# Performance work log

Measured on AMD Instinct MI355X. Metric: run time of the kernel, lower is better.

Reference implementation:

```python
import jax, jax.numpy as jnp
import numpy as np

NUM_CLASSES = 80
STRIDES = (8, 16, 32)
FEAT_HW = ((80, 80), (40, 40), (20, 20))
B = 32
MAX_GT = 60


def setup_inputs() -> dict:
    key = jax.random.key(0)
    ks = jax.random.split(key, 6)
    feats = {}
    for i, (s, (h, w)) in enumerate(zip(STRIDES, FEAT_HW)):
        feats[f"feat{s}"] = jax.random.normal(ks[i], (B, 5 + NUM_CLASSES, h, w), jnp.float32)
    u = jax.random.uniform(ks[3], (B, MAX_GT, 4), jnp.float32)
    # cx,cy in [0,640), w,h in [8,128): realistic pixel-space gt boxes for a 640x640 image
    gt_boxes = jnp.concatenate([u[..., :2] * 640.0, u[..., 2:] * 120.0 + 8.0], -1)
    gt_classes = jax.random.randint(ks[4], (B, MAX_GT), 0, NUM_CLASSES)
    num_gts = jax.random.randint(ks[5], (B,), 1, MAX_GT + 1)
    return dict(feat8=feats["feat8"], feat16=feats["feat16"], feat32=feats["feat32"],
                gt_boxes=gt_boxes, gt_classes=gt_classes, num_gts=num_gts)


def _decode(feat, stride):
    # torch get_output_and_grid: xy=(raw+grid)*stride, wh=exp(raw)*stride
    b, c, h, w = feat.shape
    yv, xv = jnp.meshgrid(jnp.arange(h), jnp.arange(w), indexing="ij")
    gx = xv.reshape(-1).astype(feat.dtype)  # [H*W]
    gy = yv.reshape(-1).astype(feat.dtype)
    out = feat.reshape(b, c, h * w).transpose(0, 2, 1)  # [B,A,C]
    xy = (out[..., :2] + jnp.stack([gx, gy], -1)[None]) * stride
    wh = jnp.exp(out[..., 2:4]) * stride
    return jnp.concatenate([xy, wh, out[..., 4:]], -1), gx, gy


def _pair_iou(a, b):
    # a: [G,4] xywh, b: [A,4] xywh -> [G,A] IoU (bboxes_iou, xyxy=False)
    tl = jnp.maximum(a[:, None, :2] - a[:, None, 2:] * 0.5, b[None, :, :2] - b[None, :, 2:] * 0.5)
    br = jnp.minimum(a[:, None, :2] + a[:, None, 2:] * 0.5, b[None, :, :2] + b[None, :, 2:] * 0.5)
    en = jnp.all(tl < br, -1)
    inter = jnp.where(en, jnp.prod(br - tl, -1), 0.0)
    area_a = jnp.prod(a[:, 2:], -1)
    area_b = jnp.prod(b[:, 2:], -1)
    return inter / (area_a[:, None] + area_b[None, :] - inter + 1e-16)


def _bce_logits(x, t):
    return jnp.maximum(x, 0.0) - x * t + jnp.log1p(jnp.exp(-jnp.abs(x)))


def _iou_loss(pred, tgt):
    # IOUloss(loss_type='iou'): 1 - iou^2, per box
    tl = jnp.maximum(pred[..., :2] - pred[..., 2:] * 0.5, tgt[..., :2] - tgt[..., 2:] * 0.5)
    br = jnp.minimum(pred[..., :2] + pred[..., 2:] * 0.5, tgt[..., :2] + tgt[..., 2:] * 0.5)
    en = jnp.all(tl < br, -1)
    inter = jnp.where(en, jnp.prod(br - tl, -1), 0.0)
    union = jnp.prod(pred[..., 2:], -1) + jnp.prod(tgt[..., 2:], -1) - inter
    iou = inter / (union + 1e-16)
    return 1.0 - iou ** 2


def _assign(boxes, cls_lo, obj_lo, gtb, gtc, vmask, cx, cy, st):
    # SimOTA per image. boxes [A,4], cls_lo [A,C], obj_lo [A], gtb [G,4], gtc [G] int,
    # vmask [G] bool (gt padding), cx/cy/st [A] anchor centers & strides.
    G, A = gtb.shape[0], boxes.shape[0]
    iou = _pair_iou(gtb, boxes)  # [G,A]
    gx, gy = gtb[:, :1], gtb[:, 1:2]
    gw, gh = gtb[:, 2:3], gtb[:, 3:4]
    in_box = ((cx[None] > gx - 0.5 * gw) & (cx[None] < gx + 0.5 * gw) &
              (cy[None] > gy - 0.5 * gh) & (cy[None] < gy + 0.5 * gh))
    R = 2.5  # center sampling radius (in strides)
    in_ctr = ((cx[None] > gx - R * st[None]) & (cx[None] < gx + R * st[None]) &
              (cy[None] > gy - R * st[None]) & (cy[None] < gy + R * st[None]))
    fg = ((in_box | in_ctr) & vmask[:, None]).any(0)  # [A] candidate anchors
    in_both = (in_box & in_ctr).astype(boxes.dtype)
    # pairwise cls cost: BCE(sqrt(sig(cls)*sig(obj)), onehot(gt_cls)).sum(-1),
    # decomposed to avoid the [G,A,C] tensor: sum_c bce0 + (bce1-bce0)[gt_cls]
    p = jnp.clip(jnp.sqrt(jax.nn.sigmoid(cls_lo) * jax.nn.sigmoid(obj_lo)[:, None]), 1e-7, 1.0 - 1e-7)
    bce1 = -jnp.log(p)          # [A,C]
    bce0 = -jnp.log(1.0 - p)    # [A,C]
    cls_cost = bce0.sum(-1)[None, :] + (bce1 - bce0)[:, gtc].T  # [G,A]
    cost = (cls_cost + 3.0 * (-jnp.log(iou + 1e-8))
            + 100000.0 * (1.0 - in_both)
            + 1e9 * (~fg)[None, :].astype(boxes.dtype)
            + 1e9 * (~vmask)[:, None].astype(boxes.dtype))
    K = 10  # n_candidate_k
    topk_ious, _ = jax.lax.top_k(iou * fg[None, :], K)
    dyn_k = jnp.maximum(topk_ious.sum(-1).astype(jnp.int32), 1)  # clamp(int(sum), min=1)
    _, pos = jax.lax.top_k(-cost, K)  # [G,K] lowest-cost anchors per gt
    sel = (jnp.arange(K)[None, :] < dyn_k[:, None]).astype(boxes.dtype)
    matching = jnp.zeros((G, A), boxes.dtype).at[jnp.arange(G)[:, None], pos].set(sel)
    matching = matching * vmask[:, None].astype(boxes.dtype)
    # resolve anchors claimed by >1 gt: keep min-cost gt
    conflict = matching.sum(0) > 1
    best_gt = jnp.argmin(cost, axis=0)  # [A]
    matching = jnp.where(conflict[None, :], jax.nn.one_hot(best_gt, G, dtype=matching.dtype).T, matching)
    fg_final = matching.sum(0) > 0  # [A]
    matched = jnp.argmax(matching, axis=0)  # [A]
    pred_iou = (matching * iou).sum(0)  # [A]
    cls_t = jax.nn.one_hot(gtc[matched], NUM_CLASSES, dtype=boxes.dtype) * pred_iou[:, None]
    reg_t = gtb[matched]
    return fg_final, cls_t, reg_t


def _forward(feat8, feat16, feat32, gt_boxes, gt_classes, num_gts):
    outs, cxs, cys, sts = [], [], [], []
    for f, s in zip((feat8, feat16, feat32), STRIDES):
        o, gx, gy = _decode(f, float(s))
        outs.append(o)
        cxs.append((gx + 0.5) * s)
        cys.append((gy + 0.5) * s)
        sts.append(jnp.full_like(gx, s))
    preds = jnp.concatenate(outs, 1)  # [B,A,5+C]
    cx = jnp.concatenate(cxs)
    cy = jnp.concatenate(cys)
    st = jnp.concatenate(sts)
    boxes = preds[..., :4]
    obj_lo = preds[..., 4]
    cls_lo = preds[..., 5:]
    vmask = jnp.arange(MAX_GT)[None, :] < num_gts[:, None]
    fg, cls_t, reg_t = jax.vmap(_assign, in_axes=(0, 0, 0, 0, 0, 0, None, None, None))(
        boxes, cls_lo, obj_lo, gt_boxes, gt_classes, vmask, cx, cy, st)
    # SimOTA assignment is no_grad in YOLOX: targets are constants wrt preds
    fg = jax.lax.stop_gradient(fg)
    cls_t = jax.lax.stop_gradient(cls_t)
    reg_t = jax.lax.stop_gradient(reg_t)
    fg_f = fg.astype(boxes.dtype)
    num_fg = jnp.maximum(fg_f.sum(), 1.0)
    loss_iou = (_iou_loss(boxes, reg_t) * fg_f).sum()
    loss_obj = _bce_logits(obj_lo, fg_f * 0.9).sum()  # obj_targets * 0.9 smoothing
    loss_cls = (_bce_logits(cls_lo, cls_t) * fg_f[..., None]).sum()
    REG_WEIGHT = 5.0
    return (REG_WEIGHT * loss_iou + loss_obj + loss_cls) / num_fg


def reference(feat8, feat16, feat32, gt_boxes, gt_classes, num_gts):
    return _forward(feat8, feat16, feat32, gt_boxes, gt_classes, num_gts)
```

## Files before the change

kernel.cpp:

```cpp
#include <hip/hip_runtime.h>

constexpr int kB = 32;
constexpr int kA = 8400;
constexpr int kG = 60;
constexpr int kC = 80;
constexpr int kK = 10;
constexpr int kNBx = (kA + 255)/256;
constexpr int kNB = kNBx * kB;

__device__ __forceinline__ float fexp(float x){ return __expf(x); }
__device__ __forceinline__ float flog(float x){ return __logf(x); }
__device__ __forceinline__ float frcp(float x){ return __builtin_amdgcn_rcpf(x); }
__device__ __forceinline__ float frsq(float x){ return __builtin_amdgcn_rsqf(x); }
__device__ __forceinline__ float fsqrt(float x){ return __builtin_amdgcn_sqrtf(x); }
__device__ __forceinline__ float fdiv(float a, float b){ return a * __builtin_amdgcn_rcpf(b); }
__device__ __forceinline__ float sigm(float x){ return frcp(1.0f + fexp(-x)); }
__device__ __forceinline__ float bce(float x, float t){
  return fmaxf(x, 0.0f) - x*t + flog(1.0f + fexp(-fabsf(x)));
}

__device__ __forceinline__ unsigned ordbits(float v){
  unsigned u = __float_as_uint(v);
  return (u & 0x80000000u) ? ~u : (u | 0x80000000u);
}
__device__ __forceinline__ float unpackf(unsigned k){
  return __uint_as_float((k & 0x80000000u) ? (k & 0x7fffffffu) : ~k);
}

struct AInfo { int x, y; float st; };
__device__ __forceinline__ AInfo ainfo(int a){
  AInfo r;
  if (a < 6400)      { r.x = a % 80;           r.y = a / 80;           r.st = 8.0f;  }
  else if (a < 8000) { int l = a-6400; r.x = l % 40; r.y = l / 40;     r.st = 16.0f; }
  else               { int l = a-8000; r.x = l % 20; r.y = l / 20;     r.st = 32.0f; }
  return r;
}

__device__ __forceinline__ float featv(const float* __restrict__ f8,
                                       const float* __restrict__ f16,
                                       const float* __restrict__ f32x,
                                       int b, int ch, int a){
  if (a < 6400) return f8 [(b*85 + ch)*6400 + a];
  if (a < 8000) return f16[(b*85 + ch)*1600 + (a - 6400)];
  return             f32x[(b*85 + ch)*400  + (a - 8000)];
}

__device__ __forceinline__ float pair_iou(float4 g, float4 p){
  float tlx = fmaxf(g.x - g.z*0.5f, p.x - p.z*0.5f);
  float tly = fmaxf(g.y - g.w*0.5f, p.y - p.w*0.5f);
  float brx = fminf(g.x + g.z*0.5f, p.x + p.z*0.5f);
  float bry = fminf(g.y + g.w*0.5f, p.y + p.w*0.5f);
  float inter = (tlx < brx && tly < bry) ? (brx-tlx)*(bry-tly) : 0.0f;
  return fdiv(inter, g.z*g.w + p.z*p.w - inter + 1e-16f);
}

__device__ __forceinline__ float cost_core(float iou, float cl, float obs, float b0sum,
                                           int a, float4 gt, int fg_a){
  AInfo ai = ainfo(a);
  float cx = ((float)ai.x + 0.5f)*ai.st;
  float cy = ((float)ai.y + 0.5f)*ai.st;
  bool in_box = (cx > gt.x - 0.5f*gt.z) && (cx < gt.x + 0.5f*gt.z)
             && (cy > gt.y - 0.5f*gt.w) && (cy < gt.y + 0.5f*gt.w);
  bool in_ctr = (cx > gt.x - 2.5f*ai.st) && (cx < gt.x + 2.5f*ai.st)
             && (cy > gt.y - 2.5f*ai.st) && (cy < gt.y + 2.5f*ai.st);
  float p = fsqrt(sigm(cl) * obs);
  p = fminf(fmaxf(p, 1e-7f), 1.0f - 1e-7f);
  float diff = -flog(p) + flog(1.0f - p);
  float c = b0sum + diff;
  c += 3.0f * (-flog(iou + 1e-8f));
  c += (in_box && in_ctr) ? 0.0f : 100000.0f;
  c += fg_a ? 0.0f : 1000000000.0f;
  return c;
}

__device__ __forceinline__ unsigned long long wave_max64(unsigned long long v){
  #pragma unroll
  for (int off = 32; off; off >>= 1){
    unsigned long long o = __shfl_xor(v, off, 64);
    if (o > v) v = o;
  }
  return v;
}

__device__ __forceinline__ void stage16(const float* g, float* l){
  __builtin_amdgcn_global_load_lds(
      (const __attribute__((address_space(1))) void*)g,
      (__attribute__((address_space(3))) void*)l, 16, 0, 0);
}
__device__ __forceinline__ void wait_vm6(int n){
  if      (n >= 6) asm volatile("s_waitcnt vmcnt(6)" ::: "memory");
  else if (n >= 4) asm volatile("s_waitcnt vmcnt(4)" ::: "memory");
  else if (n >= 2) asm volatile("s_waitcnt vmcnt(2)" ::: "memory");
  else             asm volatile("s_waitcnt vmcnt(0)" ::: "memory");
  __builtin_amdgcn_sched_barrier(0);
}

__global__ __launch_bounds__(256) void k_decode(
    const float* __restrict__ f8, const float* __restrict__ f16, const float* __restrict__ f32x,
    const float* __restrict__ gtb, const int* __restrict__ ngts,
    float* __restrict__ boxes, float* __restrict__ boxesZ,
    float* __restrict__ objl, float* __restrict__ b0s,
    float* __restrict__ bceS, float* __restrict__ obsA,
    int* __restrict__ fg, int* __restrict__ cnt, int* __restrict__ mtch){
  int b = blockIdx.y;
  int tid = threadIdx.x;
  int lane = tid & 63, wid = tid >> 6;
  int a0 = blockIdx.x*256 + tid;
  bool alive = (a0 < kA);
  int a = alive ? a0 : (kA - 1);
  __shared__ float4 sg[kG];
  __shared__ float buf[4][8][4][64];
  if (tid < kG) sg[tid] = ((const float4*)gtb)[b*kG + tid];
  int ng = ngts[b];
  __syncthreads();

  const float* base; int hw, off; float st_; int gx, gy;
  if (a < 6400)      { base=f8;   hw=6400; off=a;        st_=8.0f;  gx=off%80; gy=off/80; }
  else if (a < 8000) { base=f16;  hw=1600; off=a-6400;   st_=16.0f; gx=off%40; gy=off/40; }
  else               { base=f32x; hw=400;  off=a-8000;   st_=32.0f; gx=off%20; gy=off/20; }
  const float* p0 = base + ((size_t)b*85)*hw + off;

  int aw = blockIdx.x*256 + wid*64;
  const float* wbasep; int whw, woff;
  if (aw < 6400)      { wbasep=f8;   whw=6400; woff=aw;        }
  else if (aw < 8000) { wbasep=f16;  whw=1600; woff=aw-6400;   }
  else                { wbasep=f32x; whw=400;  woff=aw-8000;   }
  int cl4 = lane >> 4;
  int m4  = (lane & 15) << 2;
  int mo  = woff + m4; if (mo > whw - 4) mo = whw - 4;
  const float* srcb = wbasep + ((size_t)b*85 + 5)*whw + mo;
  float* ldst = &buf[wid][0][0][0];

  float t0 = p0[0];
  float t1 = p0[(size_t)hw];
  float t2 = p0[(size_t)2*hw];
  float t3 = p0[(size_t)3*hw];
  float ob = p0[(size_t)4*hw];
  __builtin_amdgcn_sched_barrier(0);
  #pragma unroll
  for (int u = 0; u < 8; ++u)
    stage16(srcb + (size_t)(4*u + cl4)*whw, ldst + u*256);
  __builtin_amdgcn_sched_barrier(0);

  float4 bx;
  bx.x = (t0 + (float)gx) * st_;
  bx.y = (t1 + (float)gy) * st_;
  bx.z = fexp(t2) * st_;
  bx.w = fexp(t3) * st_;
  float obs = sigm(ob);
  float so = fsqrt(obs);
  float cx = ((float)gx + 0.5f)*st_;
  float cy = ((float)gy + 0.5f)*st_;
  int f = 0;
  for (int g = 0; g < ng; ++g){
    float4 gt = sg[g];
    bool in_box = (cx > gt.x - 0.5f*gt.z) && (cx < gt.x + 0.5f*gt.z)
               && (cy > gt.y - 0.5f*gt.w) && (cy < gt.y + 0.5f*gt.w);
    bool in_ctr = (cx > gt.x - 2.5f*st_) && (cx < gt.x + 2.5f*st_)
               && (cy > gt.y - 2.5f*st_) && (cy < gt.y + 2.5f*st_);
    if (in_box || in_ctr){ f = 1; break; }
  }

  float s = 0.0f, sumCl = 0.0f, slogv = 0.0f;
  #pragma unroll
  for (int g = 0; g < 10; ++g){
    const int issued = (g < 6) ? (8 + 2*g) : 20;
    wait_vm6(issued - (2*g + 2));
    float cv[8];
    #pragma unroll
    for (int c = 0; c < 4; ++c) cv[c]     = buf[wid][(2*g)   & 7][c][lane];
    #pragma unroll
    for (int c = 0; c < 4; ++c) cv[4 + c] = buf[wid][(2*g+1) & 7][c][lane];
    asm volatile("s_waitcnt lgkmcnt(0)" ::: "memory");
    __builtin_amdgcn_sched_barrier(0);
    if (g < 6){
      stage16(srcb + (size_t)(4*(2*g+8) + cl4)*whw, ldst + ((2*g)   & 7)*256);
      stage16(srcb + (size_t)(4*(2*g+9) + cl4)*whw, ldst + ((2*g+1) & 7)*256);
    }
    __builtin_amdgcn_sched_barrier(0);
    float prodS = 1.0f, prodV = 1.0f;
    #pragma unroll
    for (int j = 0; j < 8; ++j){
      float c = cv[j];
      float u = fexp(-c);
      float v = 1.0f + u;
      float p = so * frsq(v);
      p = fminf(fmaxf(p, 1e-7f), 1.0f - 1e-7f);
      prodS *= (1.0f - p);
      prodV *= v;
      sumCl += c;
    }
    s -= flog(prodS);
    slogv += flog(prodV);
  }
  __builtin_amdgcn_sched_barrier(0);
  if (alive){
    int idx = b*kA + a;
    ((float4*)boxes)[idx] = bx;
    objl[idx] = ob;
    obsA[idx] = obs;
    cnt[idx] = 0;
    mtch[idx] = 0x7fffffff;
    fg[idx] = f;
    ((float4*)boxesZ)[idx] = f ? bx : make_float4(0.0f,0.0f,0.0f,0.0f);
    b0s[idx]  = s;
    bceS[idx] = sumCl + slogv;
  }
}

__global__ __launch_bounds__(256) void k_assign(
    const float* __restrict__ f8, const float* __restrict__ f16, const float* __restrict__ f32x,
    const float* __restrict__ gtb, const int* __restrict__ gtc, const int* __restrict__ ngts,
    const float* __restrict__ boxes, const float* __restrict__ boxesZ,
    const float* __restrict__ obsA, const float* __restrict__ b0s,
    const int* __restrict__ fg,
    int* __restrict__ cnt, int* __restrict__ mtch){
  int b = blockIdx.x / kG;
  int g = blockIdx.x % kG;
  if (g >= ngts[b]) return;
  int tid = threadIdx.x;
  int lane = tid & 63, wid = tid >> 6;
  float4 gt = ((const float4*)gtb)[b*kG + g];
  int cls = gtc[b*kG + g];
  const float4* bx4 = (const float4*)boxes;
  const float4* bz4 = (const float4*)boxesZ;
  const float* c8  = f8   + ((size_t)b*85 + 5 + cls)*6400;
  const float* c16 = f16  + ((size_t)b*85 + 5 + cls)*1600;
  const float* c32 = f32x + ((size_t)b*85 + 5 + cls)*400;

  __shared__ unsigned long long lds_k[4*kK];
  __shared__ int lds_cnt[4];
  __shared__ int s_dynk;

  unsigned long long k1[kK];
  #pragma unroll
  for (int i = 0; i < kK; ++i) k1[i] = 0ull;

  for (int i = tid; i < kA; i += 256){
    float4 bx = bz4[b*kA + i];
    float v = pair_iou(gt, bx);
    unsigned long long key1 = ((unsigned long long)ordbits(v) << 32) | (unsigned)(~i);
    if (key1 > k1[kK-1]){
      k1[kK-1] = key1;
      #pragma unroll
      for (int i2 = kK-1; i2 > 0; --i2)
        if (k1[i2] > k1[i2-1]){ unsigned long long t = k1[i2]; k1[i2] = k1[i2-1]; k1[i2-1] = t; }
    }
  }
  {
    unsigned long long wtop = 0ull;
    #pragma unroll
    for (int k = 0; k < kK; ++k){
      unsigned long long best = wave_max64(k1[0]);
      if (k1[0] == best){
        #pragma unroll
        for (int i2 = 0; i2 < kK-1; ++i2) k1[i2] = k1[i2+1];
        k1[kK-1] = 0ull;
      }
      if (lane == k) wtop = best;
    }
    if (lane < kK) lds_k[wid*kK + lane] = wtop;
  }
  __syncthreads();
  if (wid == 0){
    unsigned long long key = (lane < 4*kK) ? lds_k[lane] : 0ull;
    float ksum = 0.0f;
    #pragma unroll
    for (int k = 0; k < kK; ++k){
      unsigned long long best = wave_max64(key);
      if (key == best) key = 0ull;
      if (best) ksum += unpackf((unsigned)(best >> 32));
    }
    if (lane == 0) s_dynk = max((int)ksum, 1);
  }
  __syncthreads();
  int dynk = s_dynk;

  int x00,y00,nx0,n0, x01,y01,nx1,n1, x02,y02,nx2,n2;
  {
    auto rect = [&](float st, int W, int& rx0, int& ry0, int& rnx, int& rn){
      float lox = fmaxf(gt.x - 0.5f*gt.z, gt.x - 2.5f*st);
      float hix = fminf(gt.x + 0.5f*gt.z, gt.x + 2.5f*st);
      float loy = fmaxf(gt.y - 0.5f*gt.w, gt.y - 2.5f*st);
      float hiy = fminf(gt.y + 0.5f*gt.w, gt.y + 2.5f*st);
      float rs = frcp(st);
      int ax0 = max(0,   (int)floorf(lox*rs - 0.5f) - 1);
      int ax1 = min(W-1, (int)ceilf (hix*rs - 0.5f) + 1);
      int ay0 = max(0,   (int)floorf(loy*rs - 0.5f) - 1);
      int ay1 = min(W-1, (int)ceilf (hiy*rs - 0.5f) + 1);
      rx0 = ax0; ry0 = ay0;
      rnx = max(0, ax1 - ax0 + 1);
      int rny = max(0, ay1 - ay0 + 1);
      rn = rnx * rny;
    };
    rect( 8.0f, 80, x00, y00, nx0, n0);
    rect(16.0f, 40, x01, y01, nx1, n1);
    rect(32.0f, 20, x02, y02, nx2, n2);
  }
  int total = n0 + n1 + n2;

  unsigned long long ck = 0ull;
  int nvalid = 0;
  if (tid < total){
    int i = tid, ix, iy, a; float st;
    if (i < n0)           { ix = x00 + i % nx0; iy = y00 + i / nx0; a = iy*80 + ix;          st = 8.0f;  }
    else if (i < n0 + n1) { int j = i - n0;      ix = x01 + j % nx1; iy = y01 + j / nx1; a = 6400 + iy*40 + ix; st = 16.0f; }
    else                  { int j = i - n0 - n1; ix = x02 + j % nx2; iy = y02 + j / nx2; a = 8000 + iy*20 + ix; st = 32.0f; }
    float cx = ((float)ix + 0.5f)*st;
    float cy = ((float)iy + 0.5f)*st;
    bool in_box = (cx > gt.x - 0.5f*gt.z) && (cx < gt.x + 0.5f*gt.z)
               && (cy > gt.y - 0.5f*gt.w) && (cy < gt.y + 0.5f*gt.w);
    bool in_ctr = (cx > gt.x - 2.5f*st) && (cx < gt.x + 2.5f*st)
               && (cy > gt.y - 2.5f*st) && (cy < gt.y + 2.5f*st);
    if (in_box && in_ctr){
      int idx = b*kA + a;
      float4 bx = bx4[idx];
      float iou = pair_iou(gt, bx);
      float cl = (a < 6400) ? c8[a] : (a < 8000) ? c16[a-6400] : c32[a-8000];
      float c = cost_core(iou, cl, obsA[idx], b0s[idx], a, gt, 1);
      ck = ~(((unsigned long long)ordbits(c) << 32) | (unsigned)a);
      nvalid = 1;
    }
  }
  {
    unsigned long long bal = __ballot(nvalid);
    if (lane == 0) lds_cnt[wid] = __popcll(bal);
    unsigned long long wtop = 0ull;
    #pragma unroll
    for (int k = 0; k < kK; ++k){
      unsigned long long best = wave_max64(ck);
      if (ck == best) ck = 0ull;
      if (lane == k) wtop = best;
    }
    if (lane < kK) lds_k[wid*kK + lane] = wtop;
  }
  __syncthreads();
  int cnt_total = lds_cnt[0] + lds_cnt[1] + lds_cnt[2] + lds_cnt[3];
  bool fb = (dynk > cnt_total);

  if (!fb){
    if (wid == 0){
      unsigned long long key = (lane < 4*kK) ? lds_k[lane] : 0ull;
      unsigned long long mine = 0ull;
      #pragma unroll
      for (int k = 0; k < kK; ++k){
        unsigned long long best = wave_max64(key);
        if (key == best) key = 0ull;
        if (lane == k) mine = best;
      }
      if (lane < dynk && mine){
        int a = (int)((unsigned)(~mine));
        atomicAdd(&cnt[b*kA + a], 1);
        atomicMin(&mtch[b*kA + a], g);
      }
    }
    return;
  }

  __syncthreads();
  unsigned long long k2[kK];
  #pragma unroll
  for (int i = 0; i < kK; ++i) k2[i] = 0ull;
  for (int i = tid; i < kA; i += 256){
    int idx = b*kA + i;
    float4 bx = bx4[idx];
    float iou = pair_iou(gt, bx);
    int fga = fg[idx];
    float cl = (i < 6400) ? c8[i] : (i < 8000) ? c16[i-6400] : c32[i-8000];
    float c = cost_core(iou, cl, obsA[idx], b0s[idx], i, gt, fga);
    unsigned long long key2 = ~(((unsigned long long)ordbits(c) << 32) | (unsigned)i);
    if (key2 > k2[kK-1]){
      k2[kK-1] = key2;
      #pragma unroll
      for (int i2 = kK-1; i2 > 0; --i2)
        if (k2[i2] > k2[i2-1]){ unsigned long long t = k2[i2]; k2[i2] = k2[i2-1]; k2[i2-1] = t; }
    }
  }
  {
    unsigned long long wtop = 0ull;
    #pragma unroll
    for (int k = 0; k < kK; ++k){
      unsigned long long best = wave_max64(k2[0]);
      if (k2[0] == best){
        #pragma unroll
        for (int i2 = 0; i2 < kK-1; ++i2) k2[i2] = k2[i2+1];
        k2[kK-1] = 0ull;
      }
      if (lane == k) wtop = best;
    }
    if (lane < kK) lds_k[wid*kK + lane] = wtop;
  }
  __syncthreads();
  if (wid == 0){
    unsigned long long key = (lane < 4*kK) ? lds_k[lane] : 0ull;
    unsigned long long mine = 0ull;
    #pragma unroll
    for (int k = 0; k < kK; ++k){
      unsigned long long best = wave_max64(key);
      if (key == best) key = 0ull;
      if (lane == k) mine = best;
    }
    if (lane < dynk && mine){
      int a = (int)((unsigned)(~mine));
      atomicAdd(&cnt[b*kA + a], 1);
      atomicMin(&mtch[b*kA + a], g);
    }
  }
}

__global__ __launch_bounds__(256) void k_loss(
    const float* __restrict__ f8, const float* __restrict__ f16, const float* __restrict__ f32x,
    const float* __restrict__ gtb, const int* __restrict__ gtc, const int* __restrict__ ngts,
    const float* __restrict__ boxes, const float* __restrict__ objl, const float* __restrict__ b0s,
    const float* __restrict__ bceS, const float* __restrict__ obsA,
    const int* __restrict__ fg, const int* __restrict__ cnt, const int* __restrict__ mtch,
    float4* __restrict__ pacc){
  int b = blockIdx.y;
  int a = blockIdx.x*256 + threadIdx.x;
  int tid = threadIdx.x;
  __shared__ float4 sg[kG];
  __shared__ int scls[kG];
  if (tid < kG){ sg[tid] = ((const float4*)gtb)[b*kG + tid]; scls[tid] = gtc[b*kG + tid]; }
  __syncthreads();
  float li = 0.0f, lo = 0.0f, lc = 0.0f, nf = 0.0f;
  bool valid = (a < kA);
  int idx = valid ? (b*kA + a) : (b*kA);
  int c = valid ? cnt[idx] : 0;
  float ob = valid ? objl[idx] : 0.0f;
  float4 bx = valid ? ((const float4*)boxes)[idx] : make_float4(0,0,1,1);

  float fgf = 0.0f; int mg = 0;
  if (valid && c == 1){ mg = mtch[idx]; fgf = 1.0f; }
  bool need = valid && (c > 1);
  if (__any(need)){
    if (need){
      int ng = ngts[b];
      float b0 = b0s[idx];
      float obs = obsA[idx];
      int fga = fg[idx];
      float bestc = 3.0e38f; int bg = 0;
      for (int g = 0; g < ng; ++g){
        float iou = pair_iou(sg[g], bx);
        float cl = featv(f8,f16,f32x,b,5+scls[g],a);
        float cst = cost_core(iou, cl, obs, b0, a, sg[g], fga);
        if (cst < bestc){ bestc = cst; bg = g; }
      }
      mg = bg; fgf = 1.0f;
    }
  }
  if (valid){
    lo = bce(ob, fgf*0.9f);
    if (fgf > 0.0f){
      nf = 1.0f;
      float4 r = sg[mg];
      float piou = pair_iou(r, bx);
      float tlx = fmaxf(bx.x - bx.z*0.5f, r.x - r.z*0.5f);
      float tly = fmaxf(bx.y - bx.w*0.5f, r.y - r.w*0.5f);
      float brx = fminf(bx.x + bx.z*0.5f, r.x + r.z*0.5f);
      float bry = fminf(bx.y + bx.w*0.5f, r.y + r.w*0.5f);
      float inter = (tlx < brx && tly < bry) ? (brx-tlx)*(bry-tly) : 0.0f;
      float un = bx.z*bx.w + r.z*r.w - inter;
      float iou = fdiv(inter, un + 1e-16f);
      li = 1.0f - iou*iou;
      int tc = scls[mg];
      float cl_tc = featv(f8,f16,f32x,b,5+tc,a);
      lc = bceS[idx] - piou * cl_tc;
    }
  }
  for (int off = 32; off > 0; off >>= 1){
    li += __shfl_down(li, off, 64);
    lo += __shfl_down(lo, off, 64);
    lc += __shfl_down(lc, off, 64);
    nf += __shfl_down(nf, off, 64);
  }
  __shared__ float4 wred[4];
  int wid = tid >> 6;
  if ((tid & 63) == 0) wred[wid] = make_float4(li, lo, lc, nf);
  __syncthreads();
  if (tid == 0){
    float4 t = wred[0];
    for (int w = 1; w < 4; ++w){
      float4 o = wred[w];
      t.x += o.x; t.y += o.y; t.z += o.z; t.w += o.w;
    }
    pacc[blockIdx.y * gridDim.x + blockIdx.x] = t;
  }
}

__global__ __launch_bounds__(256) void k_final(
    const float4* __restrict__ pacc, float* __restrict__ out){
  int tid = threadIdx.x;
  float li = 0.0f, lo = 0.0f, lc = 0.0f, nf = 0.0f;
  for (int i = tid; i < kNB; i += 256){
    float4 p = pacc[i];
    li += p.x; lo += p.y; lc += p.z; nf += p.w;
  }
  for (int off = 32; off > 0; off >>= 1){
    li += __shfl_down(li, off, 64);
    lo += __shfl_down(lo, off, 64);
    lc += __shfl_down(lc, off, 64);
    nf += __shfl_down(nf, off, 64);
  }
  __shared__ float4 wred[4];
  int wid = tid >> 6;
  if ((tid & 63) == 0) wred[wid] = make_float4(li, lo, lc, nf);
  __syncthreads();
  if (tid == 0){
    float4 t = wred[0];
    for (int w = 1; w < 4; ++w){
      float4 o = wred[w];
      t.x += o.x; t.y += o.y; t.z += o.z; t.w += o.w;
    }
    out[0] = (5.0f*t.x + t.y + t.z) * frcp(fmaxf(t.w, 1.0f));
  }
}

extern "C" void kernel_launch(void* const* d_in, const int* in_sizes, int n_in,
                              void* d_out, int out_size, void* d_ws, size_t ws_size,
                              hipStream_t stream) {
  (void)in_sizes; (void)n_in; (void)out_size; (void)ws_size;
  const float* f8   = (const float*)d_in[0];
  const float* f16  = (const float*)d_in[1];
  const float* f32x = (const float*)d_in[2];
  const float* gtb  = (const float*)d_in[3];
  const int*   gtc  = (const int*)d_in[4];
  const int*   ngts = (const int*)d_in[5];
  float* out = (float*)d_out;

  const size_t BA = (size_t)kB*kA;
  float* ws     = (float*)d_ws;
  float* boxes  = ws;
  float* boxesZ = boxes  + BA*4;
  float* objl   = boxesZ + BA*4;
  float* b0s    = objl   + BA;
  float* bceS   = b0s    + BA;
  float* obsA   = bceS   + BA;
  int*   fg     = (int*)(obsA + BA);
  int*   cnt    = fg  + BA;
  int*   mtch   = cnt + BA;
  float4* pacc  = (float4*)(mtch + BA);

  dim3 gBA(kNBx, kB);
  k_decode<<<gBA, dim3(256), 0, stream>>>(f8,f16,f32x,gtb,ngts,boxes,boxesZ,objl,b0s,bceS,obsA,fg,cnt,mtch);
  k_assign<<<dim3(kB*kG), dim3(256), 0, stream>>>(f8,f16,f32x,gtb,gtc,ngts,boxes,boxesZ,obsA,b0s,fg,cnt,mtch);
  k_loss<<<gBA, dim3(256), 0, stream>>>(f8,f16,f32x,gtb,gtc,ngts,boxes,objl,b0s,bceS,obsA,fg,cnt,mtch,pacc);
  k_final<<<dim3(1), dim3(256), 0, stream>>>(pacc, out);
}
```

Before: 199.3 us.

## Stage class logits block-wide with full-row loads and barriers

Restructures the decode kernel's class-logit staging so each wave loads a whole 256-anchor row per class (1 KB contiguous) into a block-shared LDS ring, instead of each wave loading its own 64-anchor slice of four classes. Blocks that fall entirely inside one feature level use this path and synchronise the ring with block barriers. The tail block spanning levels falls back to direct strided global loads. The aim is wider, more coalesced DMA transfers into LDS, at the cost of two block barriers per stage and a slow scalar path for the last block.

```diff
diff --git a/kernel.cpp b/kernel.cpp
--- a/kernel.cpp
+++ b/kernel.cpp
@@ -94,6 +94,11 @@
   else             asm volatile("s_waitcnt vmcnt(0)" ::: "memory");
   __builtin_amdgcn_sched_barrier(0);
 }
+__device__ __forceinline__ void block_bar(){
+  __builtin_amdgcn_sched_barrier(0);
+  __builtin_amdgcn_s_barrier();
+  __builtin_amdgcn_sched_barrier(0);
+}
 
 __global__ __launch_bounds__(256) void k_decode(
     const float* __restrict__ f8, const float* __restrict__ f16, const float* __restrict__ f32x,
@@ -109,7 +114,7 @@
   bool alive = (a0 < kA);
   int a = alive ? a0 : (kA - 1);
   __shared__ float4 sg[kG];
-  __shared__ float buf[4][8][4][64];
+  __shared__ float buf[8][4][256];
   if (tid < kG) sg[tid] = ((const float4*)gtb)[b*kG + tid];
   int ng = ngts[b];
   __syncthreads();
@@ -119,17 +124,6 @@
   else if (a < 8000) { base=f16;  hw=1600; off=a-6400;   st_=16.0f; gx=off%40; gy=off/40; }
   else               { base=f32x; hw=400;  off=a-8000;   st_=32.0f; gx=off%20; gy=off/20; }
   const float* p0 = base + ((size_t)b*85)*hw + off;
-
-  int aw = blockIdx.x*256 + wid*64;
-  const float* wbasep; int whw, woff;
-  if (aw < 6400)      { wbasep=f8;   whw=6400; woff=aw;        }
-  else if (aw < 8000) { wbasep=f16;  whw=1600; woff=aw-6400;   }
-  else                { wbasep=f32x; whw=400;  woff=aw-8000;   }
-  int cl4 = lane >> 4;
-  int m4  = (lane & 15) << 2;
-  int mo  = woff + m4; if (mo > whw - 4) mo = whw - 4;
-  const float* srcb = wbasep + ((size_t)b*85 + 5)*whw + mo;
-  float* ldst = &buf[wid][0][0][0];
 
   float t0 = p0[0];
   float t1 = p0[(size_t)hw];
@@ -137,9 +131,21 @@
   float t3 = p0[(size_t)3*hw];
   float ob = p0[(size_t)4*hw];
   __builtin_amdgcn_sched_barrier(0);
-  #pragma unroll
-  for (int u = 0; u < 8; ++u)
-    stage16(srcb + (size_t)(4*u + cl4)*whw, ldst + u*256);
+
+  bool pure = (blockIdx.x < 31);
+  const float* csrc = nullptr;
+  size_t lhw = 0;
+  if (pure){
+    int ab = blockIdx.x*256;
+    const float* lv; int lh, lo_;
+    if (ab < 6400){ lv = f8;  lh = 6400; lo_ = ab; }
+    else          { lv = f16; lh = 1600; lo_ = ab - 6400; }
+    lhw = (size_t)lh;
+    csrc = lv + ((size_t)b*85 + 5)*lh + lo_ + lane*4;
+    #pragma unroll
+    for (int u = 0; u < 8; ++u)
+      stage16(csrc + (size_t)(4*u + wid)*lhw, &buf[u][wid][0]);
+  }
   __builtin_amdgcn_sched_barrier(0);
 
   float4 bx;
@@ -162,36 +168,59 @@
   }
 
   float s = 0.0f, sumCl = 0.0f, slogv = 0.0f;
-  #pragma unroll
-  for (int g = 0; g < 10; ++g){
-    const int issued = (g < 6) ? (8 + 2*g) : 20;
-    wait_vm6(issued - (2*g + 2));
-    float cv[8];
-    #pragma unroll
-    for (int c = 0; c < 4; ++c) cv[c]     = buf[wid][(2*g)   & 7][c][lane];
-    #pragma unroll
-    for (int c = 0; c < 4; ++c) cv[4 + c] = buf[wid][(2*g+1) & 7][c][lane];
-    asm volatile("s_waitcnt lgkmcnt(0)" ::: "memory");
-    __builtin_amdgcn_sched_barrier(0);
-    if (g < 6){
-      stage16(srcb + (size_t)(4*(2*g+8) + cl4)*whw, ldst + ((2*g)   & 7)*256);
-      stage16(srcb + (size_t)(4*(2*g+9) + cl4)*whw, ldst + ((2*g+1) & 7)*256);
-    }
-    __builtin_amdgcn_sched_barrier(0);
-    float prodS = 1.0f, prodV = 1.0f;
-    #pragma unroll
-    for (int j = 0; j < 8; ++j){
-      float c = cv[j];
-      float u = fexp(-c);
-      float v = 1.0f + u;
-      float p = so * frsq(v);
-      p = fminf(fmaxf(p, 1e-7f), 1.0f - 1e-7f);
-      prodS *= (1.0f - p);
-      prodV *= v;
-      sumCl += c;
-    }
-    s -= flog(prodS);
-    slogv += flog(prodV);
+  if (pure){
+    #pragma unroll
+    for (int g = 0; g < 10; ++g){
+      const int allowed = (g < 6) ? 6 : (18 - 2*g);
+      wait_vm6(allowed);
+      block_bar();
+      float cv[8];
+      #pragma unroll
+      for (int c = 0; c < 4; ++c) cv[c]     = buf[(2*g)   & 7][c][tid];
+      #pragma unroll
+      for (int c = 0; c < 4; ++c) cv[4 + c] = buf[(2*g+1) & 7][c][tid];
+      asm volatile("s_waitcnt lgkmcnt(0)" ::: "memory");
+      __builtin_amdgcn_sched_barrier(0);
+      block_bar();
+      if (g < 6){
+        stage16(csrc + (size_t)(4*(2*g+8) + wid)*lhw, &buf[(2*g)   & 7][wid][0]);
+        stage16(csrc + (size_t)(4*(2*g+9) + wid)*lhw, &buf[(2*g+1) & 7][wid][0]);
+      }
+      __builtin_amdgcn_sched_barrier(0);
+      float prodS = 1.0f, prodV = 1.0f;
+      #pragma unroll
+      for (int j = 0; j < 8; ++j){
+        float c = cv[j];
+        float u = fexp(-c);
+        float v = 1.0f + u;
+        float p = so * frsq(v);
+        p = fminf(fmaxf(p, 1e-7f), 1.0f - 1e-7f);
+        prodS *= (1.0f - p);
+        prodV *= v;
+        sumCl += c;
+      }
+      s -= flog(prodS);
+      slogv += flog(prodV);
+    }
+  } else {
+    const float* pc = p0 + (size_t)5*hw;
+    #pragma unroll 1
+    for (int grp = 0; grp < kC/8; ++grp){
+      float prodS = 1.0f, prodV = 1.0f;
+      #pragma unroll
+      for (int j = 0; j < 8; ++j){
+        float c = pc[(size_t)(grp*8 + j)*hw];
+        float u = fexp(-c);
+        float v = 1.0f + u;
+        float p = so * frsq(v);
+        p = fminf(fmaxf(p, 1e-7f), 1.0f - 1e-7f);
+        prodS *= (1.0f - p);
+        prodV *= v;
+        sumCl += c;
+      }
+      s -= flog(prodS);
+      slogv += flog(prodV);
+    }
   }
   __builtin_amdgcn_sched_barrier(0);
   if (alive){
```

Result: no change. 198.9 us (-0.2%).
